# Performance work log

Hardware: AMD Instinct MI355X
Metric: run time of the kernel (lower is better)

## Reference

```python
import jax, jax.numpy as jnp
import numpy as np

H = 1024       # hidden_size
NH = 16        # num_attention_heads
HD = H // NH   # attention_head_size = 64


def setup_inputs() -> dict:
    key = jax.random.key(0)
    ks = jax.random.split(key, 9)
    s = 1.0 / np.sqrt(H)
    return {
        "hidden_states": jax.random.normal(ks[0], (2, 2048, H), dtype=jnp.float32),
        "Wq": jax.random.uniform(ks[1], (H, H), jnp.float32, -s, s),
        "bq": jax.random.uniform(ks[2], (H,), jnp.float32, -s, s),
        "Wk": jax.random.uniform(ks[3], (H, H), jnp.float32, -s, s),
        "bk": jax.random.uniform(ks[4], (H,), jnp.float32, -s, s),
        "Wv": jax.random.uniform(ks[5], (H, H), jnp.float32, -s, s),
        "bv": jax.random.uniform(ks[6], (H,), jnp.float32, -s, s),
        "Wo": jax.random.uniform(ks[7], (H, H), jnp.float32, -s, s),
        "bo": jax.random.uniform(ks[8], (H,), jnp.float32, -s, s),
    }


def _heads(x, B, S):
    # [B, S, H] -> [B, NH, S, HD]
    return x.reshape(B, S, NH, HD).transpose(0, 2, 1, 3)


def reference(hidden_states, Wq, bq, Wk, bk, Wv, bv, Wo, bo):
    B, S, _ = hidden_states.shape
    q = _heads(hidden_states @ Wq.T + bq, B, S)
    k = _heads(hidden_states @ Wk.T + bk, B, S)
    v = _heads(hidden_states @ Wv.T + bv, B, S)
    scores = jnp.einsum('bhqd,bhkd->bhqk', q, k) / jnp.sqrt(jnp.float32(HD))
    probs = jax.nn.softmax(scores, axis=-1)
    ctx = jnp.einsum('bhqk,bhkd->bhqd', probs, v)  # [B, NH, S, HD]
    ctx = ctx.transpose(0, 2, 1, 3).reshape(B, S, H)
    return ctx @ Wo.T + bo
```

## Files before the change

kernel.cpp:

```cpp
#include <hip/hip_runtime.h>
#include <stdint.h>


#define HH 1024
#define NHEAD 16
#define HDIM 64
#define SEQ 2048
#define NB 2
#define MTOT (NB * SEQ)
#define QSCALE 0.1803368801111204f
#define BK 32

typedef unsigned short u16;
typedef __attribute__((ext_vector_type(8))) short bf16x8;
typedef __attribute__((ext_vector_type(4))) float f32x4;

static __device__ __forceinline__ float exp2_raw(float x) {
  float r; asm("v_exp_f32 %0, %1" : "=v"(r) : "v"(x)); return r;
}
static __device__ __forceinline__ uint32_t cvtpk_bf16(float lo, float hi) {
  uint32_t r; asm("v_cvt_pk_bf16_f32 %0, %1, %2" : "=v"(r) : "v"(lo), "v"(hi)); return r;
}
static __device__ __forceinline__ void gload16(const u16* g, u16* l) {
  __builtin_amdgcn_global_load_lds(
      (const __attribute__((address_space(1))) uint32_t*)(const void*)g,
      (__attribute__((address_space(3))) uint32_t*)(void*)l, 16, 0, 0);
}
#define VMW(N) asm volatile("s_waitcnt vmcnt(" #N ")" ::: "memory")
static __device__ __forceinline__ void bar() {
  asm volatile("" ::: "memory");
  __builtin_amdgcn_s_barrier();
  asm volatile("" ::: "memory");
}

#define SWZ(row, col) (((row) * 64) + ((col) ^ (((row) & 7) << 3)))

__global__ void cvt_kernel(const float* __restrict__ src, u16* __restrict__ dst, int n4) {
  int i = blockIdx.x * 256 + threadIdx.x;
  if (i >= n4) return;
  float4 v = reinterpret_cast<const float4*>(src)[i];
  uint2 o;
  o.x = cvtpk_bf16(v.x, v.y);
  o.y = cvtpk_bf16(v.z, v.w);
  reinterpret_cast<uint2*>(dst)[i] = o;
}

__global__ void cvtw_kernel(const float* __restrict__ s0, const float* __restrict__ s1,
                            const float* __restrict__ s2, const float* __restrict__ s3,
                            u16* __restrict__ dst, int n4) {
  const float* s = (blockIdx.y == 0) ? s0 : (blockIdx.y == 1) ? s1 : (blockIdx.y == 2) ? s2 : s3;
  int i = blockIdx.x * 256 + threadIdx.x;
  if (i >= n4) return;
  float4 v = reinterpret_cast<const float4*>(s)[i];
  uint2 o;
  o.x = cvtpk_bf16(v.x, v.y);
  o.y = cvtpk_bf16(v.z, v.w);
  reinterpret_cast<uint2*>(dst + (size_t)blockIdx.y * HH * HH)[i] = o;
}

__global__ __launch_bounds__(512, 4)
void gemm128_kernel(const u16* __restrict__ A, const u16* __restrict__ W,
                    const float* __restrict__ bq, const float* __restrict__ bk,
                    const float* __restrict__ bv, const float* __restrict__ bo,
                    u16* __restrict__ outQ, u16* __restrict__ outK, u16* __restrict__ outVT,
                    float* __restrict__ outF, int isQKV)
{
  const int tid  = threadIdx.x;
  const int lane = tid & 63, wave = tid >> 6;
  const int wm = wave >> 1, wn = wave & 1;
  const int l15 = lane & 15, l4 = lane >> 4;
  const int brow = blockIdx.x * 128, bcol = blockIdx.y * 128;

  __shared__ __align__(16) u16 lA[4][128 * BK];
  __shared__ __align__(16) u16 lB[4][128 * BK];

  const int sr = wave * 16 + (lane >> 2);
  const int sc = (lane & 3) ^ ((sr >> 1) & 3);
  const u16* gA = A + (size_t)(brow + sr) * HH + sc * 8;
  const u16* gB = W + (size_t)(bcol + sr) * HH + sc * 8;

  int aoff[2], boff[4];
#pragma unroll
  for (int mr = 0; mr < 2; ++mr) {
    int r = wm * 32 + mr * 16 + l15;
    aoff[mr] = r * BK + ((l4 ^ ((r >> 1) & 3)) * 8);
  }
#pragma unroll
  for (int nr = 0; nr < 4; ++nr) {
    int r = wn * 64 + nr * 16 + l15;
    boff[nr] = r * BK + ((l4 ^ ((r >> 1) & 3)) * 8);
  }

  f32x4 acc[2][4];
#pragma unroll
  for (int mr = 0; mr < 2; ++mr)
#pragma unroll
    for (int nr = 0; nr < 4; ++nr) acc[mr][nr] = (f32x4){0.f, 0.f, 0.f, 0.f};

#pragma unroll
  for (int t = 0; t < 3; ++t) {
    gload16(gA + t * BK, (u16*)((char*)&lA[t][0] + wave * 1024));
    gload16(gB + t * BK, (u16*)((char*)&lB[t][0] + wave * 1024));
  }

  for (int k = 0; k < 32; ++k) {
    const int rem = 31 - k;
    if (rem >= 2)      VMW(4);
    else if (rem == 1) VMW(2);
    else               VMW(0);
    bar();

    const int s = k & 3, tt = (k + 3) & 3;
    if (k + 3 < 32) {
      gload16(gA + (k + 3) * BK, (u16*)((char*)&lA[tt][0] + wave * 1024));
      gload16(gB + (k + 3) * BK, (u16*)((char*)&lB[tt][0] + wave * 1024));
    }

    const u16* sA = &lA[s][0];
    const u16* sB = &lB[s][0];
    bf16x8 a[2], b[4];
#pragma unroll
    for (int nr = 0; nr < 4; ++nr) b[nr] = *reinterpret_cast<const bf16x8*>(sB + boff[nr]);
#pragma unroll
    for (int mr = 0; mr < 2; ++mr) a[mr] = *reinterpret_cast<const bf16x8*>(sA + aoff[mr]);

    __builtin_amdgcn_s_setprio(1);
#pragma unroll
    for (int mr = 0; mr < 2; ++mr)
#pragma unroll
      for (int nr = 0; nr < 4; ++nr)
        acc[mr][nr] = __builtin_amdgcn_mfma_f32_16x16x32_bf16(a[mr], b[nr], acc[mr][nr], 0, 0, 0);
    __builtin_amdgcn_s_setprio(0);
  }

  const int mode = isQKV ? (bcol >> 10) : 3;
#pragma unroll
  for (int mr = 0; mr < 2; ++mr) {
    int m0 = brow + wm * 32 + mr * 16 + l4 * 4;
    int bb = m0 >> 11, s0 = m0 & (SEQ - 1);
#pragma unroll
    for (int nr = 0; nr < 4; ++nr) {
      int n = bcol + wn * 64 + nr * 16 + l15;
      if (mode == 3) {
        float bias_n = bo[n];
#pragma unroll
        for (int t = 0; t < 4; ++t)
          outF[(size_t)(m0 + t) * HH + n] = acc[mr][nr][t] + bias_n;
      } else {
        int nn = n & (HH - 1);
        int h = nn >> 6, d = nn & (HDIM - 1);
        float bias_n = (mode == 0) ? bq[nn] : (mode == 1) ? bk[nn] : bv[nn];
        if (mode == 2) {
          int p0 = (s0 & ~31) | (((s0 >> 2) & 3) << 3) | (((s0 >> 4) & 1) << 2);
          uint2 pk4;
          pk4.x = cvtpk_bf16(acc[mr][nr][0] + bias_n, acc[mr][nr][1] + bias_n);
          pk4.y = cvtpk_bf16(acc[mr][nr][2] + bias_n, acc[mr][nr][3] + bias_n);
          *reinterpret_cast<uint2*>(&outVT[((size_t)(bb * NHEAD + h) * HDIM + d) * SEQ + p0]) = pk4;
        } else {
          u16* dst = (mode == 0) ? outQ : outK;
          float sc2 = (mode == 0) ? QSCALE : 1.0f;
          uint32_t r01 = cvtpk_bf16((acc[mr][nr][0] + bias_n) * sc2, (acc[mr][nr][1] + bias_n) * sc2);
          uint32_t r23 = cvtpk_bf16((acc[mr][nr][2] + bias_n) * sc2, (acc[mr][nr][3] + bias_n) * sc2);
          size_t base = ((size_t)(bb * NHEAD + h) * SEQ + s0) * HDIM + d;
          dst[base]            = (u16)r01;
          dst[base + HDIM]     = (u16)(r01 >> 16);
          dst[base + 2 * HDIM] = (u16)r23;
          dst[base + 3 * HDIM] = (u16)(r23 >> 16);
        }
      }
    }
  }
}

__global__ __launch_bounds__(256)
void attn_kernel(const u16* __restrict__ Qh, const u16* __restrict__ Kh,
                 const u16* __restrict__ VTh, u16* __restrict__ CTX)
{
  const int head = blockIdx.x;
  const int qb   = blockIdx.y;
  const int tid  = threadIdx.x;
  const int lane = tid & 63, wave = tid >> 6;
  const int l15 = lane & 15, l4 = lane >> 4;

  __shared__ __align__(16) u16 lK[2][64 * 64];
  __shared__ __align__(16) u16 lV[2][64 * 64];

  const u16* Qg = Qh + ((size_t)head * SEQ + qb * 128 + wave * 32) * HDIM;
  const u16* Kg = Kh + (size_t)head * SEQ * HDIM;
  const u16* Vg = VTh + (size_t)head * HDIM * SEQ;

  int er[2], ec[2];
#pragma unroll
  for (int p = 0; p < 2; ++p) { int e = p * 256 + tid; er[p] = e >> 3; ec[p] = (e & 7) * 8; }

  bf16x8 qf[2][2];
#pragma unroll
  for (int g = 0; g < 2; ++g)
#pragma unroll
    for (int kk = 0; kk < 2; ++kk)
      qf[g][kk] = *reinterpret_cast<const bf16x8*>(&Qg[(g * 16 + l15) * HDIM + kk * 32 + l4 * 8]);

#pragma unroll
  for (int p = 0; p < 2; ++p) {
    *reinterpret_cast<int4*>(&lK[0][SWZ(er[p], ec[p])]) =
        *reinterpret_cast<const int4*>(&Kg[er[p] * 64 + ec[p]]);
    *reinterpret_cast<int4*>(&lV[0][SWZ(er[p], ec[p])]) =
        *reinterpret_cast<const int4*>(&Vg[(size_t)er[p] * SEQ + ec[p]]);
  }
  __syncthreads();

  union { uint32_t u[4]; bf16x8 v; } ones;
#pragma unroll
  for (int t = 0; t < 4; ++t) ones.u[t] = 0x3F803F80u;

  f32x4 accO[2][4];
  f32x4 accS[2];
#pragma unroll
  for (int g = 0; g < 2; ++g) {
#pragma unroll
    for (int dj = 0; dj < 4; ++dj) accO[g][dj] = (f32x4){0.f, 0.f, 0.f, 0.f};
    accS[g] = (f32x4){0.f, 0.f, 0.f, 0.f};
  }

  for (int kb = 0; kb < SEQ / 64; ++kb) {
    const int cur = kb & 1;
    const bool pre = (kb + 1 < SEQ / 64);
    int4 kreg[2], vreg[2];
    if (pre) {
#pragma unroll
      for (int p = 0; p < 2; ++p) {
        kreg[p] = *reinterpret_cast<const int4*>(&Kg[(size_t)((kb + 1) * 64 + er[p]) * HDIM + ec[p]]);
        vreg[p] = *reinterpret_cast<const int4*>(&Vg[(size_t)er[p] * SEQ + (kb + 1) * 64 + ec[p]]);
      }
    }

    bf16x8 kf[2][4];
#pragma unroll
    for (int kk = 0; kk < 2; ++kk)
#pragma unroll
      for (int kj = 0; kj < 4; ++kj)
        kf[kk][kj] = *reinterpret_cast<const bf16x8*>(&lK[cur][SWZ(kj * 16 + l15, kk * 32 + l4 * 8)]);

    uint32_t pk[2][4][2];
#pragma unroll
    for (int g = 0; g < 2; ++g) {
      f32x4 sf[4];
#pragma unroll
      for (int kj = 0; kj < 4; ++kj) sf[kj] = (f32x4){0.f, 0.f, 0.f, 0.f};
      __builtin_amdgcn_s_setprio(1);
#pragma unroll
      for (int kk = 0; kk < 2; ++kk)
#pragma unroll
        for (int kj = 0; kj < 4; ++kj)
          sf[kj] = __builtin_amdgcn_mfma_f32_16x16x32_bf16(kf[kk][kj], qf[g][kk], sf[kj], 0, 0, 0);
      __builtin_amdgcn_s_setprio(0);
#pragma unroll
      for (int kj = 0; kj < 4; ++kj) {
        float p0 = exp2_raw(sf[kj][0]);
        float p1 = exp2_raw(sf[kj][1]);
        float p2 = exp2_raw(sf[kj][2]);
        float p3 = exp2_raw(sf[kj][3]);
        pk[g][kj][0] = cvtpk_bf16(p0, p1);
        pk[g][kj][1] = cvtpk_bf16(p2, p3);
      }
    }

#pragma unroll
    for (int kk = 0; kk < 2; ++kk) {
      bf16x8 vf[4];
#pragma unroll
      for (int dj = 0; dj < 4; ++dj)
        vf[dj] = *reinterpret_cast<const bf16x8*>(&lV[cur][SWZ(dj * 16 + l15, kk * 32 + l4 * 8)]);
      __builtin_amdgcn_s_setprio(1);
#pragma unroll
      for (int g = 0; g < 2; ++g) {
        union { uint32_t u[4]; bf16x8 v; } pf;
        pf.u[0] = pk[g][2 * kk][0];     pf.u[1] = pk[g][2 * kk][1];
        pf.u[2] = pk[g][2 * kk + 1][0]; pf.u[3] = pk[g][2 * kk + 1][1];
#pragma unroll
        for (int dj = 0; dj < 4; ++dj)
          accO[g][dj] = __builtin_amdgcn_mfma_f32_16x16x32_bf16(vf[dj], pf.v, accO[g][dj], 0, 0, 0);
        accS[g] = __builtin_amdgcn_mfma_f32_16x16x32_bf16(ones.v, pf.v, accS[g], 0, 0, 0);
      }
      __builtin_amdgcn_s_setprio(0);
    }

    if (pre) {
#pragma unroll
      for (int p = 0; p < 2; ++p) {
        *reinterpret_cast<int4*>(&lK[cur ^ 1][SWZ(er[p], ec[p])]) = kreg[p];
        *reinterpret_cast<int4*>(&lV[cur ^ 1][SWZ(er[p], ec[p])]) = vreg[p];
      }
      __syncthreads();
    }
  }

  const int bb = head >> 4, h = head & (NHEAD - 1);
#pragma unroll
  for (int g = 0; g < 2; ++g) {
    const int sq = qb * 128 + wave * 32 + g * 16 + l15;
    float inv = 1.0f / accS[g][0];
#pragma unroll
    for (int dj = 0; dj < 4; ++dj) {
      uint2 o;
      o.x = cvtpk_bf16(accO[g][dj][0] * inv, accO[g][dj][1] * inv);
      o.y = cvtpk_bf16(accO[g][dj][2] * inv, accO[g][dj][3] * inv);
      *reinterpret_cast<uint2*>(&CTX[((size_t)(bb * SEQ + sq)) * HH + h * HDIM + dj * 16 + l4 * 4]) = o;
    }
  }
}

extern "C" void kernel_launch(void* const* d_in, const int* in_sizes, int n_in,
                              void* d_out, int out_size, void* d_ws, size_t ws_size,
                              hipStream_t stream) {
  const float* hs = (const float*)d_in[0];
  const float* Wq = (const float*)d_in[1];
  const float* bq = (const float*)d_in[2];
  const float* Wk = (const float*)d_in[3];
  const float* bk = (const float*)d_in[4];
  const float* Wv = (const float*)d_in[5];
  const float* bv = (const float*)d_in[6];
  const float* Wo = (const float*)d_in[7];
  const float* bo = (const float*)d_in[8];
  float* out = (float*)d_out;

  char* ws = (char*)d_ws;
  u16* Xb   = (u16*)(ws);
  u16* Wall = (u16*)(ws + ((size_t)8 << 20));
  u16* Qh   = (u16*)(ws + ((size_t)16 << 20));
  u16* Kh   = (u16*)(ws + ((size_t)24 << 20));
  u16* VT   = (u16*)(ws + ((size_t)32 << 20));
  u16* CT   = Xb;

  int n4x = MTOT * HH / 4;
  cvt_kernel<<<dim3((n4x + 255) / 256), 256, 0, stream>>>(hs, Xb, n4x);
  int n4w = HH * HH / 4;
  cvtw_kernel<<<dim3((n4w + 255) / 256, 4), 256, 0, stream>>>(Wq, Wk, Wv, Wo, Wall, n4w);

  gemm128_kernel<<<dim3(MTOT / 128, 3 * HH / 128), 512, 0, stream>>>(
      Xb, Wall, bq, bk, bv, bo, Qh, Kh, VT, nullptr, 1);

  attn_kernel<<<dim3(NB * NHEAD, SEQ / 128), 256, 0, stream>>>(Qh, Kh, VT, CT);

  gemm128_kernel<<<dim3(MTOT / 128, HH / 128), 512, 0, stream>>>(
      CT, Wall + (size_t)3 * HH * HH, bq, bk, bv, bo, nullptr, nullptr, nullptr, out, 0);
}
```

Measured before the change: 125.9 us.

## Split attention over key range and merge the two conversion kernels

The attention kernel now splits the key sequence into two halves across a third grid dimension. Each half writes unnormalized fp32 partial outputs and row sums to workspace, and a new combine kernel adds them, normalizes and converts to bf16. This doubles the block count (512 to 1024) to fill more CUs and sets a 4-blocks-per-CU launch bound. The cost is about 33 MB of extra fp32 traffic plus an extra launch. The combine is only exact because the softmax carries no running max, so both halves share the same scale. The input and weight conversion kernels are also fused into one launch.

```diff
diff --git a/kernel.cpp b/kernel.cpp
--- a/kernel.cpp
+++ b/kernel.cpp
@@ -35,27 +35,24 @@
 
 #define SWZ(row, col) (((row) * 64) + ((col) ^ (((row) & 7) << 3)))
 
-__global__ void cvt_kernel(const float* __restrict__ src, u16* __restrict__ dst, int n4) {
+__global__ void cvt_all_kernel(const float* __restrict__ hs,
+                               const float* __restrict__ w0, const float* __restrict__ w1,
+                               const float* __restrict__ w2, const float* __restrict__ w3,
+                               u16* __restrict__ Xb, u16* __restrict__ Wall) {
+  const int z = blockIdx.y;
   int i = blockIdx.x * 256 + threadIdx.x;
-  if (i >= n4) return;
-  float4 v = reinterpret_cast<const float4*>(src)[i];
-  uint2 o;
-  o.x = cvtpk_bf16(v.x, v.y);
-  o.y = cvtpk_bf16(v.z, v.w);
-  reinterpret_cast<uint2*>(dst)[i] = o;
-}
-
-__global__ void cvtw_kernel(const float* __restrict__ s0, const float* __restrict__ s1,
-                            const float* __restrict__ s2, const float* __restrict__ s3,
-                            u16* __restrict__ dst, int n4) {
-  const float* s = (blockIdx.y == 0) ? s0 : (blockIdx.y == 1) ? s1 : (blockIdx.y == 2) ? s2 : s3;
-  int i = blockIdx.x * 256 + threadIdx.x;
+  const float* s; u16* d; int n4;
+  if (z == 0) { s = hs; d = Xb; n4 = MTOT * HH / 4; }
+  else {
+    s = (z == 1) ? w0 : (z == 2) ? w1 : (z == 3) ? w2 : w3;
+    d = Wall + (size_t)(z - 1) * HH * HH; n4 = HH * HH / 4;
+  }
   if (i >= n4) return;
   float4 v = reinterpret_cast<const float4*>(s)[i];
   uint2 o;
   o.x = cvtpk_bf16(v.x, v.y);
   o.y = cvtpk_bf16(v.z, v.w);
-  reinterpret_cast<uint2*>(dst + (size_t)blockIdx.y * HH * HH)[i] = o;
+  reinterpret_cast<uint2*>(d)[i] = o;
 }
 
 __global__ __launch_bounds__(512, 4)
@@ -172,12 +169,16 @@
   }
 }
 
-__global__ __launch_bounds__(256)
+template<int NSPLIT>
+__global__ __launch_bounds__(256, 4)
 void attn_kernel(const u16* __restrict__ Qh, const u16* __restrict__ Kh,
-                 const u16* __restrict__ VTh, u16* __restrict__ CTX)
+                 const u16* __restrict__ VTh, u16* __restrict__ CTX,
+                 float* __restrict__ P, float* __restrict__ L)
 {
+  constexpr int NT = (SEQ / 64) / NSPLIT;
   const int head = blockIdx.x;
   const int qb   = blockIdx.y;
+  const int ks   = blockIdx.z;
   const int tid  = threadIdx.x;
   const int lane = tid & 63, wave = tid >> 6;
   const int l15 = lane & 15, l4 = lane >> 4;
@@ -186,8 +187,8 @@
   __shared__ __align__(16) u16 lV[2][64 * 64];
 
   const u16* Qg = Qh + ((size_t)head * SEQ + qb * 128 + wave * 32) * HDIM;
-  const u16* Kg = Kh + (size_t)head * SEQ * HDIM;
-  const u16* Vg = VTh + (size_t)head * HDIM * SEQ;
+  const u16* Kg = Kh + (size_t)head * SEQ * HDIM + (size_t)ks * (SEQ / NSPLIT) * HDIM;
+  const u16* Vg = VTh + (size_t)head * HDIM * SEQ + (size_t)ks * (SEQ / NSPLIT);
 
   int er[2], ec[2];
 #pragma unroll
@@ -222,9 +223,9 @@
     accS[g] = (f32x4){0.f, 0.f, 0.f, 0.f};
   }
 
-  for (int kb = 0; kb < SEQ / 64; ++kb) {
+  for (int kb = 0; kb < NT; ++kb) {
     const int cur = kb & 1;
-    const bool pre = (kb + 1 < SEQ / 64);
+    const bool pre = (kb + 1 < NT);
     int4 kreg[2], vreg[2];
     if (pre) {
 #pragma unroll
@@ -299,15 +300,41 @@
 #pragma unroll
   for (int g = 0; g < 2; ++g) {
     const int sq = qb * 128 + wave * 32 + g * 16 + l15;
-    float inv = 1.0f / accS[g][0];
-#pragma unroll
-    for (int dj = 0; dj < 4; ++dj) {
-      uint2 o;
-      o.x = cvtpk_bf16(accO[g][dj][0] * inv, accO[g][dj][1] * inv);
-      o.y = cvtpk_bf16(accO[g][dj][2] * inv, accO[g][dj][3] * inv);
-      *reinterpret_cast<uint2*>(&CTX[((size_t)(bb * SEQ + sq)) * HH + h * HDIM + dj * 16 + l4 * 4]) = o;
-    }
-  }
+    const size_t row = (size_t)bb * SEQ + sq;
+    if constexpr (NSPLIT == 1) {
+      float inv = 1.0f / accS[g][0];
+#pragma unroll
+      for (int dj = 0; dj < 4; ++dj) {
+        uint2 o;
+        o.x = cvtpk_bf16(accO[g][dj][0] * inv, accO[g][dj][1] * inv);
+        o.y = cvtpk_bf16(accO[g][dj][2] * inv, accO[g][dj][3] * inv);
+        *reinterpret_cast<uint2*>(&CTX[row * HH + h * HDIM + dj * 16 + l4 * 4]) = o;
+      }
+    } else {
+      float* Pp = P + (size_t)ks * (MTOT * HH) + row * HH + h * HDIM;
+#pragma unroll
+      for (int dj = 0; dj < 4; ++dj) {
+        float4 o = {accO[g][dj][0], accO[g][dj][1], accO[g][dj][2], accO[g][dj][3]};
+        *reinterpret_cast<float4*>(&Pp[dj * 16 + l4 * 4]) = o;
+      }
+      if (l4 == 0) L[(size_t)ks * (MTOT * NHEAD) + row * NHEAD + h] = accS[g][0];
+    }
+  }
+}
+
+__global__ void combine_kernel(const float* __restrict__ P, const float* __restrict__ L,
+                               u16* __restrict__ CTX) {
+  int i = blockIdx.x * 256 + threadIdx.x;
+  float4 p0 = reinterpret_cast<const float4*>(P)[i];
+  float4 p1 = reinterpret_cast<const float4*>(P + (size_t)MTOT * HH)[i];
+  int hd = (i * 4) & (HH - 1), row = (i * 4) >> 10;
+  int h = hd >> 6;
+  float l = L[row * NHEAD + h] + L[MTOT * NHEAD + row * NHEAD + h];
+  float inv = 1.0f / l;
+  uint2 o;
+  o.x = cvtpk_bf16((p0.x + p1.x) * inv, (p0.y + p1.y) * inv);
+  o.y = cvtpk_bf16((p0.z + p1.z) * inv, (p0.w + p1.w) * inv);
+  reinterpret_cast<uint2*>(CTX)[i] = o;
 }
 
 extern "C" void kernel_launch(void* const* d_in, const int* in_sizes, int n_in,
@@ -331,16 +358,24 @@
   u16* Kh   = (u16*)(ws + ((size_t)24 << 20));
   u16* VT   = (u16*)(ws + ((size_t)32 << 20));
   u16* CT   = Xb;
-
-  int n4x = MTOT * HH / 4;
-  cvt_kernel<<<dim3((n4x + 255) / 256), 256, 0, stream>>>(hs, Xb, n4x);
-  int n4w = HH * HH / 4;
-  cvtw_kernel<<<dim3((n4w + 255) / 256, 4), 256, 0, stream>>>(Wq, Wk, Wv, Wo, Wall, n4w);
+  float* P  = (float*)(ws + ((size_t)40 << 20));
+  float* L  = (float*)(ws + ((size_t)74 << 20));
+  const bool use_split = (ws_size >= ((size_t)76 << 20));
+
+  cvt_all_kernel<<<dim3(MTOT * HH / 4 / 256, 5), 256, 0, stream>>>(
+      hs, Wq, Wk, Wv, Wo, Xb, Wall);
 
   gemm128_kernel<<<dim3(MTOT / 128, 3 * HH / 128), 512, 0, stream>>>(
       Xb, Wall, bq, bk, bv, bo, Qh, Kh, VT, nullptr, 1);
 
-  attn_kernel<<<dim3(NB * NHEAD, SEQ / 128), 256, 0, stream>>>(Qh, Kh, VT, CT);
+  if (use_split) {
+    attn_kernel<2><<<dim3(NB * NHEAD, SEQ / 128, 2), 256, 0, stream>>>(
+        Qh, Kh, VT, nullptr, P, L);
+    combine_kernel<<<dim3(MTOT * HH / 4 / 256), 256, 0, stream>>>(P, L, CT);
+  } else {
+    attn_kernel<1><<<dim3(NB * NHEAD, SEQ / 128, 1), 256, 0, stream>>>(
+        Qh, Kh, VT, CT, nullptr, nullptr);
+  }
 
   gemm128_kernel<<<dim3(MTOT / 128, HH / 128), 512, 0, stream>>>(
       CT, Wall + (size_t)3 * HH * HH, bq, bk, bv, bo, nullptr, nullptr, nullptr, out, 0);
```

New measurement: 131.6 us. 4.6% more time.

## Split QKV GEMM into 4-wave kernel with larger per-wave tiles and merge conversion launches

Applied to the files above, without the earlier changes.

Introduces a dedicated QKV projection kernel using 256 threads where each wave computes a 64x64 sub-tile (4x4 MFMAs per k-step), with a 3-slot LDS ring buffer and two-ahead prefetch. It aims for more MFMA work per LDS fragment load and higher register reuse. The output projection keeps the original 512-thread kernel. The two fp32-to-bf16 conversion launches are merged into one grid to save a launch. The larger accumulator set raises register pressure and lowers occupancy, which is why launch bounds drop to 3 blocks per unit.

```diff
diff --git a/kernel.cpp b/kernel.cpp
--- a/kernel.cpp
+++ b/kernel.cpp
@@ -35,35 +35,31 @@
 
 #define SWZ(row, col) (((row) * 64) + ((col) ^ (((row) & 7) << 3)))
 
-__global__ void cvt_kernel(const float* __restrict__ src, u16* __restrict__ dst, int n4) {
+__global__ void cvt_all_kernel(const float* __restrict__ hs,
+                               const float* __restrict__ w0, const float* __restrict__ w1,
+                               const float* __restrict__ w2, const float* __restrict__ w3,
+                               u16* __restrict__ Xb, u16* __restrict__ Wall) {
+  const int z = blockIdx.y;
   int i = blockIdx.x * 256 + threadIdx.x;
-  if (i >= n4) return;
-  float4 v = reinterpret_cast<const float4*>(src)[i];
-  uint2 o;
-  o.x = cvtpk_bf16(v.x, v.y);
-  o.y = cvtpk_bf16(v.z, v.w);
-  reinterpret_cast<uint2*>(dst)[i] = o;
-}
-
-__global__ void cvtw_kernel(const float* __restrict__ s0, const float* __restrict__ s1,
-                            const float* __restrict__ s2, const float* __restrict__ s3,
-                            u16* __restrict__ dst, int n4) {
-  const float* s = (blockIdx.y == 0) ? s0 : (blockIdx.y == 1) ? s1 : (blockIdx.y == 2) ? s2 : s3;
-  int i = blockIdx.x * 256 + threadIdx.x;
+  const float* s; u16* d; int n4;
+  if (z == 0) { s = hs; d = Xb; n4 = MTOT * HH / 4; }
+  else {
+    s = (z == 1) ? w0 : (z == 2) ? w1 : (z == 3) ? w2 : w3;
+    d = Wall + (size_t)(z - 1) * HH * HH; n4 = HH * HH / 4;
+  }
   if (i >= n4) return;
   float4 v = reinterpret_cast<const float4*>(s)[i];
   uint2 o;
   o.x = cvtpk_bf16(v.x, v.y);
   o.y = cvtpk_bf16(v.z, v.w);
-  reinterpret_cast<uint2*>(dst + (size_t)blockIdx.y * HH * HH)[i] = o;
-}
-
-__global__ __launch_bounds__(512, 4)
-void gemm128_kernel(const u16* __restrict__ A, const u16* __restrict__ W,
-                    const float* __restrict__ bq, const float* __restrict__ bk,
-                    const float* __restrict__ bv, const float* __restrict__ bo,
-                    u16* __restrict__ outQ, u16* __restrict__ outK, u16* __restrict__ outVT,
-                    float* __restrict__ outF, int isQKV)
+  reinterpret_cast<uint2*>(d)[i] = o;
+}
+
+__global__ __launch_bounds__(256, 3)
+void gemm_qkv_kernel(const u16* __restrict__ A, const u16* __restrict__ W,
+                     const float* __restrict__ bq, const float* __restrict__ bk,
+                     const float* __restrict__ bv,
+                     u16* __restrict__ outQ, u16* __restrict__ outK, u16* __restrict__ outVT)
 {
   const int tid  = threadIdx.x;
   const int lane = tid & 63, wave = tid >> 6;
@@ -71,6 +67,109 @@
   const int l15 = lane & 15, l4 = lane >> 4;
   const int brow = blockIdx.x * 128, bcol = blockIdx.y * 128;
 
+  __shared__ __align__(16) u16 lA[3][128 * BK];
+  __shared__ __align__(16) u16 lB[3][128 * BK];
+
+  const int sr = wave * 16 + (lane >> 2);
+  const int sc = (lane & 3) ^ ((sr >> 1) & 3);
+  const u16* gA0 = A + (size_t)(brow + sr) * HH + sc * 8;
+  const u16* gA1 = A + (size_t)(brow + sr + 64) * HH + sc * 8;
+  const u16* gB0 = W + (size_t)(bcol + sr) * HH + sc * 8;
+  const u16* gB1 = W + (size_t)(bcol + sr + 64) * HH + sc * 8;
+
+#define STAGEQ(slot, kt)                                                      \
+  { gload16(gA0 + (kt) * BK, (u16*)((char*)&lA[slot][0] + wave * 1024));      \
+    gload16(gA1 + (kt) * BK, (u16*)((char*)&lA[slot][0] + 4096 + wave * 1024)); \
+    gload16(gB0 + (kt) * BK, (u16*)((char*)&lB[slot][0] + wave * 1024));      \
+    gload16(gB1 + (kt) * BK, (u16*)((char*)&lB[slot][0] + 4096 + wave * 1024)); }
+
+  int aoff[4], boff[4];
+#pragma unroll
+  for (int mr = 0; mr < 4; ++mr) {
+    int r = wm * 64 + mr * 16 + l15;
+    aoff[mr] = r * BK + ((l4 ^ ((r >> 1) & 3)) * 8);
+  }
+#pragma unroll
+  for (int nr = 0; nr < 4; ++nr) {
+    int r = wn * 64 + nr * 16 + l15;
+    boff[nr] = r * BK + ((l4 ^ ((r >> 1) & 3)) * 8);
+  }
+
+  f32x4 acc[4][4];
+#pragma unroll
+  for (int mr = 0; mr < 4; ++mr)
+#pragma unroll
+    for (int nr = 0; nr < 4; ++nr) acc[mr][nr] = (f32x4){0.f, 0.f, 0.f, 0.f};
+
+  STAGEQ(0, 0);
+  STAGEQ(1, 1);
+
+  for (int k = 0; k < 32; ++k) {
+    if (k < 31) VMW(4); else VMW(0);
+    bar();
+
+    if (k + 2 < 32) STAGEQ((k + 2) % 3, k + 2);
+
+    const u16* sA = &lA[k % 3][0];
+    const u16* sB = &lB[k % 3][0];
+    bf16x8 a[4], b[4];
+#pragma unroll
+    for (int nr = 0; nr < 4; ++nr) b[nr] = *reinterpret_cast<const bf16x8*>(sB + boff[nr]);
+#pragma unroll
+    for (int mr = 0; mr < 4; ++mr) a[mr] = *reinterpret_cast<const bf16x8*>(sA + aoff[mr]);
+
+    __builtin_amdgcn_s_setprio(1);
+#pragma unroll
+    for (int mr = 0; mr < 4; ++mr)
+#pragma unroll
+      for (int nr = 0; nr < 4; ++nr)
+        acc[mr][nr] = __builtin_amdgcn_mfma_f32_16x16x32_bf16(a[mr], b[nr], acc[mr][nr], 0, 0, 0);
+    __builtin_amdgcn_s_setprio(0);
+  }
+#undef STAGEQ
+
+  const int mode = bcol >> 10;
+#pragma unroll
+  for (int mr = 0; mr < 4; ++mr) {
+    int m0 = brow + wm * 64 + mr * 16 + l4 * 4;
+    int bb = m0 >> 11, s0 = m0 & (SEQ - 1);
+#pragma unroll
+    for (int nr = 0; nr < 4; ++nr) {
+      int n = bcol + wn * 64 + nr * 16 + l15;
+      int nn = n & (HH - 1);
+      int h = nn >> 6, d = nn & (HDIM - 1);
+      float bias_n = (mode == 0) ? bq[nn] : (mode == 1) ? bk[nn] : bv[nn];
+      if (mode == 2) {
+        int p0 = (s0 & ~31) | (((s0 >> 2) & 3) << 3) | (((s0 >> 4) & 1) << 2);
+        uint2 pk4;
+        pk4.x = cvtpk_bf16(acc[mr][nr][0] + bias_n, acc[mr][nr][1] + bias_n);
+        pk4.y = cvtpk_bf16(acc[mr][nr][2] + bias_n, acc[mr][nr][3] + bias_n);
+        *reinterpret_cast<uint2*>(&outVT[((size_t)(bb * NHEAD + h) * HDIM + d) * SEQ + p0]) = pk4;
+      } else {
+        u16* dst = (mode == 0) ? outQ : outK;
+        float sc2 = (mode == 0) ? QSCALE : 1.0f;
+        uint32_t r01 = cvtpk_bf16((acc[mr][nr][0] + bias_n) * sc2, (acc[mr][nr][1] + bias_n) * sc2);
+        uint32_t r23 = cvtpk_bf16((acc[mr][nr][2] + bias_n) * sc2, (acc[mr][nr][3] + bias_n) * sc2);
+        size_t base = ((size_t)(bb * NHEAD + h) * SEQ + s0) * HDIM + d;
+        dst[base]            = (u16)r01;
+        dst[base + HDIM]     = (u16)(r01 >> 16);
+        dst[base + 2 * HDIM] = (u16)r23;
+        dst[base + 3 * HDIM] = (u16)(r23 >> 16);
+      }
+    }
+  }
+}
+
+__global__ __launch_bounds__(512, 4)
+void gemm_o_kernel(const u16* __restrict__ A, const u16* __restrict__ W,
+                   const float* __restrict__ bo, float* __restrict__ outF)
+{
+  const int tid  = threadIdx.x;
+  const int lane = tid & 63, wave = tid >> 6;
+  const int wm = wave >> 1, wn = wave & 1;
+  const int l15 = lane & 15, l4 = lane >> 4;
+  const int brow = blockIdx.x * 128, bcol = blockIdx.y * 128;
+
   __shared__ __align__(16) u16 lA[4][128 * BK];
   __shared__ __align__(16) u16 lB[4][128 * BK];
 
@@ -133,41 +232,16 @@
     __builtin_amdgcn_s_setprio(0);
   }
 
-  const int mode = isQKV ? (bcol >> 10) : 3;
 #pragma unroll
   for (int mr = 0; mr < 2; ++mr) {
     int m0 = brow + wm * 32 + mr * 16 + l4 * 4;
-    int bb = m0 >> 11, s0 = m0 & (SEQ - 1);
 #pragma unroll
     for (int nr = 0; nr < 4; ++nr) {
       int n = bcol + wn * 64 + nr * 16 + l15;
-      if (mode == 3) {
-        float bias_n = bo[n];
-#pragma unroll
-        for (int t = 0; t < 4; ++t)
-          outF[(size_t)(m0 + t) * HH + n] = acc[mr][nr][t] + bias_n;
-      } else {
-        int nn = n & (HH - 1);
-        int h = nn >> 6, d = nn & (HDIM - 1);
-        float bias_n = (mode == 0) ? bq[nn] : (mode == 1) ? bk[nn] : bv[nn];
-        if (mode == 2) {
-          int p0 = (s0 & ~31) | (((s0 >> 2) & 3) << 3) | (((s0 >> 4) & 1) << 2);
-          uint2 pk4;
-          pk4.x = cvtpk_bf16(acc[mr][nr][0] + bias_n, acc[mr][nr][1] + bias_n);
-          pk4.y = cvtpk_bf16(acc[mr][nr][2] + bias_n, acc[mr][nr][3] + bias_n);
-          *reinterpret_cast<uint2*>(&outVT[((size_t)(bb * NHEAD + h) * HDIM + d) * SEQ + p0]) = pk4;
-        } else {
-          u16* dst = (mode == 0) ? outQ : outK;
-          float sc2 = (mode == 0) ? QSCALE : 1.0f;
-          uint32_t r01 = cvtpk_bf16((acc[mr][nr][0] + bias_n) * sc2, (acc[mr][nr][1] + bias_n) * sc2);
-          uint32_t r23 = cvtpk_bf16((acc[mr][nr][2] + bias_n) * sc2, (acc[mr][nr][3] + bias_n) * sc2);
-          size_t base = ((size_t)(bb * NHEAD + h) * SEQ + s0) * HDIM + d;
-          dst[base]            = (u16)r01;
-          dst[base + HDIM]     = (u16)(r01 >> 16);
-          dst[base + 2 * HDIM] = (u16)r23;
-          dst[base + 3 * HDIM] = (u16)(r23 >> 16);
-        }
-      }
+      float bias_n = bo[n];
+#pragma unroll
+      for (int t = 0; t < 4; ++t)
+        outF[(size_t)(m0 + t) * HH + n] = acc[mr][nr][t] + bias_n;
     }
   }
 }
@@ -332,16 +406,14 @@
   u16* VT   = (u16*)(ws + ((size_t)32 << 20));
   u16* CT   = Xb;
 
-  int n4x = MTOT * HH / 4;
-  cvt_kernel<<<dim3((n4x + 255) / 256), 256, 0, stream>>>(hs, Xb, n4x);
-  int n4w = HH * HH / 4;
-  cvtw_kernel<<<dim3((n4w + 255) / 256, 4), 256, 0, stream>>>(Wq, Wk, Wv, Wo, Wall, n4w);
-
-  gemm128_kernel<<<dim3(MTOT / 128, 3 * HH / 128), 512, 0, stream>>>(
-      Xb, Wall, bq, bk, bv, bo, Qh, Kh, VT, nullptr, 1);
+  cvt_all_kernel<<<dim3(MTOT * HH / 4 / 256, 5), 256, 0, stream>>>(
+      hs, Wq, Wk, Wv, Wo, Xb, Wall);
+
+  gemm_qkv_kernel<<<dim3(MTOT / 128, 3 * HH / 128), 256, 0, stream>>>(
+      Xb, Wall, bq, bk, bv, Qh, Kh, VT);
 
   attn_kernel<<<dim3(NB * NHEAD, SEQ / 128), 256, 0, stream>>>(Qh, Kh, VT, CT);
 
-  gemm128_kernel<<<dim3(MTOT / 128, HH / 128), 512, 0, stream>>>(
-      CT, Wall + (size_t)3 * HH * HH, bq, bk, bv, bo, nullptr, nullptr, nullptr, out, 0);
-}
+  gemm_o_kernel<<<dim3(MTOT / 128, HH / 128), 512, 0, stream>>>(
+      CT, Wall + (size_t)3 * HH * HH, bo, out);
+}
```

Result: faster. 111.9 us (-11.1%).
